# Optimization experiments

Hardware: AMD Instinct MI355X
Metric: run time of the kernel (lower is better)

## Reference

```python
import jax, jax.numpy as jnp
import numpy as np

K = 3       # kernel size
PAD = 1     # k // 2
S = 1       # stride
EPS = 1e-5  # BatchNorm eps


def setup_inputs() -> dict:
    key = jax.random.key(0)
    ks = jax.random.split(key, 7)
    B, C1, C2, H, W = 4, 256, 256, 80, 80
    x = jax.random.normal(ks[0], (B, C1, H, W), dtype=jnp.float32)
    # offset/mask conv params (orig inits these to zero; use small random so
    # the deformable sampling path is actually exercised)
    w_off = jax.random.normal(ks[1], (3 * K * K, C1, K, K), dtype=jnp.float32) * 0.01
    b_off = jax.random.normal(ks[2], (3 * K * K,), dtype=jnp.float32) * 0.01
    weight = jax.random.normal(ks[3], (C2, C1, K, K), dtype=jnp.float32) * 0.05
    bias = jax.random.normal(ks[4], (C2,), dtype=jnp.float32) * 0.05
    gamma = jnp.ones((C2,), dtype=jnp.float32)
    beta = jnp.zeros((C2,), dtype=jnp.float32)
    return {"x": x, "w_off": w_off, "b_off": b_off, "weight": weight,
            "bias": bias, "gamma": gamma, "beta": beta}


def _elastic_head(x, w_off, b_off, weight, bias, gamma, beta):
    B, C, H, W = x.shape
    K2 = K * K
    # offset/mask predictor conv (stride 1, SAME padding -> output H x W)
    off_out = jax.lax.conv_general_dilated(
        x, w_off, (S, S), 'SAME',
        dimension_numbers=('NCHW', 'OIHW', 'NCHW')) + b_off[None, :, None, None]
    o1, o2, m = off_out[:, :K2], off_out[:, K2:2 * K2], off_out[:, 2 * K2:]
    mask = jax.nn.sigmoid(m)                                   # [B,K2,H,W]
    # torchvision layout: channel 2p = dy_p, 2p+1 = dx_p
    off = jnp.concatenate([o1, o2], axis=1).reshape(B, K2, 2, H, W)
    dy, dx = off[:, :, 0], off[:, :, 1]                        # [B,K2,H,W]
    # base sampling grid per kernel tap
    ii, jj = jnp.meshgrid(jnp.arange(K), jnp.arange(K), indexing='ij')
    ii = ii.reshape(K2)
    jj = jj.reshape(K2)
    base_y = (jnp.arange(H)[None, :] * S - PAD + ii[:, None]).astype(x.dtype)  # [K2,H]
    base_x = (jnp.arange(W)[None, :] * S - PAD + jj[:, None]).astype(x.dtype)  # [K2,W]
    ys = dy + base_y[None, :, :, None]                         # [B,K2,H,W]
    xs = dx + base_x[None, :, None, :]
    y0 = jnp.floor(ys)
    x0 = jnp.floor(xs)
    wy = ys - y0
    wx = xs - x0
    y0i = y0.astype(jnp.int32)
    x0i = x0.astype(jnp.int32)
    y1i = y0i + 1
    x1i = x0i + 1
    x_flat = x.reshape(B, C, H * W)

    def gather(yy, xx):
        valid = ((yy >= 0) & (yy < H) & (xx >= 0) & (xx < W)).astype(x.dtype)
        idx = jnp.clip(yy, 0, H - 1) * W + jnp.clip(xx, 0, W - 1)
        g = jax.vmap(lambda xf, ix: xf[:, ix])(x_flat, idx.reshape(B, -1))
        return g.reshape(B, C, K2, H, W) * valid[:, None]

    # bilinear sample with zero padding outside, accumulate corners
    patches = (gather(y0i, x0i) * ((1 - wy) * (1 - wx))[:, None]
               + gather(y0i, x1i) * ((1 - wy) * wx)[:, None]
               + gather(y1i, x0i) * (wy * (1 - wx))[:, None]
               + gather(y1i, x1i) * (wy * wx)[:, None])       # [B,C,K2,H,W]
    patches = patches * mask[:, None]                          # modulation
    # implicit GEMM of deform_conv2d
    out = jnp.einsum('bcphw,ocp->bohw', patches,
                     weight.reshape(weight.shape[0], C, K2)) + bias[None, :, None, None]
    # BatchNorm2d (training-mode batch stats, biased variance) + SiLU
    mean = out.mean(axis=(0, 2, 3))
    var = out.var(axis=(0, 2, 3))
    xn = (out - mean[None, :, None, None]) * jax.lax.rsqrt(var + EPS)[None, :, None, None]
    y_bn = xn * gamma[None, :, None, None] + beta[None, :, None, None]
    return y_bn * jax.nn.sigmoid(y_bn)


def reference(x, w_off, b_off, weight, bias, gamma, beta):
    return _elastic_head(x, w_off, b_off, weight, bias, gamma, beta)
```

## Files before the change

### kernel.cpp

```cpp
#include <hip/hip_runtime.h>
#include <math.h>

constexpr int Hc = 80, Wc = 80, Bn = 4, C1 = 256, C2 = 256;
constexpr int HWn = Hc * Wc;
constexpr int NPIX = Bn * HWn;
constexpr int OFFC = 27;
constexpr int KK   = 2304;

typedef short bf16x8 __attribute__((ext_vector_type(8)));
typedef float f32x4  __attribute__((ext_vector_type(4)));

__device__ __forceinline__ unsigned f2bf(float f) {
    unsigned u = __float_as_uint(f);
    return (u + 0x7FFF + ((u >> 16) & 1)) >> 16;
}

__device__ __forceinline__ unsigned packhi2(float v0, float v1) {
    unsigned h;
    asm("v_cvt_pk_bf16_f32 %0, %1, %2" : "=v"(h) : "v"(v0), "v"(v1));
    return h;
}

__device__ __forceinline__ void ub4(uint2 u, float f[4]) {
    f[0] = __uint_as_float(u.x << 16);
    f[1] = __uint_as_float(u.x & 0xffff0000u);
    f[2] = __uint_as_float(u.y << 16);
    f[3] = __uint_as_float(u.y & 0xffff0000u);
}

__global__ __launch_bounds__(256) void k_wprep(const float* __restrict__ weight,
                                               unsigned short* __restrict__ wB1)
{
    int e = blockIdx.x * 256 + threadIdx.x;
    int kin = e & 7;
    int oc  = (e >> 3) & 255;
    int kg  = (e >> 11) & 3;
    int s   = e >> 13;
    int p   = s >> 3, cc = s & 7;
    float w = weight[((size_t)oc * C1 + cc * 32 + kg * 8 + kin) * 9 + p];
    wB1[e] = (unsigned short)f2bf(w);
}

__global__ __launch_bounds__(256) void k_wobprep(const float* __restrict__ w_off,
                                                 unsigned short* __restrict__ wOB)
{
    int e = blockIdx.x * 256 + threadIdx.x;
    int k  = e & 31;
    int oc = (e >> 5) & 31;
    int s  = e >> 10;
    int p  = s >> 3, cc = s & 7;
    float v = 0.f;
    if (oc < 27) v = w_off[((size_t)oc * C1 + cc * 32 + k) * 9 + p];
    wOB[e] = (unsigned short)f2bf(v);
}

__global__ __launch_bounds__(256) void k_xtrans(const float* __restrict__ x,
                                                unsigned short* __restrict__ xTb)
{
    __shared__ float tile[32][33];
    int bid = blockIdx.x;
    int ct  = bid & 7;
    int hwt = (bid >> 3) % 200;
    int b   = bid / 1600;
    int c0  = ct * 32, hw0 = hwt * 32;
    int tid = threadIdx.x;
    int col = tid & 31, rw = tid >> 5;
    const float* xb = x + (size_t)b * C1 * HWn;
    #pragma unroll
    for (int k = 0; k < 4; ++k) {
        int r = rw + k * 8;
        tile[r][col] = xb[(size_t)(c0 + r) * HWn + hw0 + col];
    }
    __syncthreads();
    unsigned short* xob = xTb + ((size_t)b * HWn + hw0) * C1 + c0;
    #pragma unroll
    for (int k = 0; k < 4; ++k) {
        int r = rw + k * 8;
        xob[(size_t)r * C1 + col] = (unsigned short)f2bf(tile[col][r]);
    }
}

__global__ __launch_bounds__(256) void k_offmfma(const unsigned short* __restrict__ xTb,
                                                 const unsigned short* __restrict__ wOB,
                                                 const float* __restrict__ b_off,
                                                 float* __restrict__ off)
{
    int t  = threadIdx.x;
    int wv = t >> 6, lane = t & 63;
    int li = lane & 15, kg = lane >> 4;
    int mi = wv & 1;
    int nj = wv >> 1;

    int mtile = ((blockIdx.x & 7) * 100) + (blockIdx.x >> 3);
    int m0  = mtile * 32;
    int b   = m0 / HWn;
    int hw0 = m0 - b * HWn;
    int pxl = hw0 + mi * 16 + li;
    int h = pxl / Wc, w = pxl - h * Wc;

    const unsigned short* xb = xTb + (size_t)b * HWn * C1;

    f32x4 acc = (f32x4){0.f, 0.f, 0.f, 0.f};
    #pragma unroll
    for (int p = 0; p < 9; ++p) {
        int dh = p / 3 - 1, dw = p % 3 - 1;
        int hh = h + dh, ww = w + dw;
        bool valid = (hh >= 0 && hh < Hc && ww >= 0 && ww < Wc);
        int hwp = valid ? (hh * Wc + ww) : 0;
        const unsigned short* arow = xb + (size_t)hwp * C1 + kg * 8;
        const unsigned short* brow = wOB + ((size_t)(p * 8) * 32 + nj * 16 + li) * 32 + kg * 8;
        #pragma unroll
        for (int cc = 0; cc < 8; ++cc) {
            uint4 av = *(const uint4*)(arow + cc * 32);
            if (!valid) av = make_uint4(0, 0, 0, 0);
            uint4 bv = *(const uint4*)(brow + cc * 1024);
            acc = __builtin_amdgcn_mfma_f32_16x16x32_bf16(
                __builtin_bit_cast(bf16x8, av), __builtin_bit_cast(bf16x8, bv), acc, 0, 0, 0);
        }
    }
    int oc = nj * 16 + li;
    if (oc < OFFC) {
        float bs = b_off[oc];
        float4 v;
        v.x = acc[0] + bs; v.y = acc[1] + bs; v.z = acc[2] + bs; v.w = acc[3] + bs;
        int hwd = hw0 + mi * 16 + kg * 4;
        *(float4*)&off[((size_t)b * OFFC + oc) * HWn + hwd] = v;
    }
}

__global__ __launch_bounds__(256) void k_meta(const float* __restrict__ off,
                                              int* __restrict__ crdbuf,
                                              float4* __restrict__ w4buf)
{
    int pair = blockIdx.x * 256 + threadIdx.x;
    int px = pair / 9, p = pair - px * 9;
    int b  = px / HWn, hw = px - b * HWn;
    int h = hw / Wc, w = hw - h * Wc;
    int ii = p / 3, jj = p - ii * 3;

    const float* ob = off + (size_t)b * OFFC * HWn + hw;
    float dy = ob[(2 * p) * HWn];
    float dx = ob[(2 * p + 1) * HWn];
    float mv = ob[(18 + p) * HWn];
    float mask = 1.0f / (1.0f + expf(-mv));
    float ys = dy + (float)(h - 1 + ii);
    float xsv = dx + (float)(w - 1 + jj);
    float y0f = floorf(ys), x0f = floorf(xsv);
    float wy = ys - y0f, wx = xsv - x0f;
    int y0 = (int)y0f, x0 = (int)x0f;
    int y1 = y0 + 1, x1 = x0 + 1;
    float vy0 = (y0 >= 0 && y0 < Hc) ? 1.f : 0.f;
    float vy1 = (y1 >= 0 && y1 < Hc) ? 1.f : 0.f;
    float vx0 = (x0 >= 0 && x0 < Wc) ? 1.f : 0.f;
    float vx1 = (x1 >= 0 && x1 < Wc) ? 1.f : 0.f;
    float4 wv;
    wv.x = mask * (1.f - wy) * (1.f - wx) * vy0 * vx0;
    wv.y = mask * (1.f - wy) * wx         * vy0 * vx1;
    wv.z = mask * wy         * (1.f - wx) * vy1 * vx0;
    wv.w = mask * wy         * wx         * vy1 * vx1;
    int cy0 = min(max(y0, 0), Hc - 1), cy1 = min(max(y1, 0), Hc - 1);
    int cx0 = min(max(x0, 0), Wc - 1), cx1 = min(max(x1, 0), Wc - 1);
    crdbuf[pair] = cy0 | (cy1 << 8) | (cx0 << 16) | (cx1 << 24);
    w4buf[pair]  = wv;
}

__global__ __launch_bounds__(256) void k_gather(const unsigned short* __restrict__ xTb,
                                                const int* __restrict__ crdbuf,
                                                const float4* __restrict__ w4buf,
                                                unsigned short* __restrict__ Ahi)
{
    int t   = threadIdx.x;
    int wv  = t >> 6, l = t & 63;
    int xcd = blockIdx.x & 7;
    int blk = blockIdx.x >> 3;
    int wgl = (xcd * 400 + blk) * 4 + wv;
    int base = wgl * 18;

    #pragma unroll 2
    for (int i = 0; i < 18; ++i) {
        int pair = base + i;
        int px = pair / 9, p = pair - px * 9;
        int b  = px / HWn;
        int crd = crdbuf[pair];
        float4 w4 = w4buf[pair];
        int cy0 = crd & 255, cy1 = (crd >> 8) & 255;
        int cx0 = (crd >> 16) & 255, cx1 = (crd >> 24) & 255;
        const unsigned short* xt = xTb + (size_t)b * HWn * C1;
        uint2 u00 = ((const uint2*)&xt[(size_t)(cy0 * Wc + cx0) * C1])[l];
        uint2 u01 = ((const uint2*)&xt[(size_t)(cy0 * Wc + cx1) * C1])[l];
        uint2 u10 = ((const uint2*)&xt[(size_t)(cy1 * Wc + cx0) * C1])[l];
        uint2 u11 = ((const uint2*)&xt[(size_t)(cy1 * Wc + cx1) * C1])[l];
        float f00[4], f01[4], f10[4], f11[4];
        ub4(u00, f00); ub4(u01, f01); ub4(u10, f10); ub4(u11, f11);
        float v0 = fmaf(w4.x, f00[0], fmaf(w4.y, f01[0], fmaf(w4.z, f10[0], w4.w * f11[0])));
        float v1 = fmaf(w4.x, f00[1], fmaf(w4.y, f01[1], fmaf(w4.z, f10[1], w4.w * f11[1])));
        float v2 = fmaf(w4.x, f00[2], fmaf(w4.y, f01[2], fmaf(w4.z, f10[2], w4.w * f11[2])));
        float v3 = fmaf(w4.x, f00[3], fmaf(w4.y, f01[3], fmaf(w4.z, f10[3], w4.w * f11[3])));
        unsigned h0 = packhi2(v0, v1), h1 = packhi2(v2, v3);
        int s = p * 8 + (l >> 3);
        size_t aidx = ((size_t)s * NPIX + px) * 32 + 4 * (l & 7);
        *(uint2*)&Ahi[aidx] = make_uint2(h0, h1);
    }
}

__global__ __launch_bounds__(256) void k_dmfma(const unsigned short* __restrict__ Ahi,
                                               const unsigned short* __restrict__ wB1,
                                               const float* __restrict__ bias,
                                               float* __restrict__ out)
{
    __shared__ float Tb[32 * 33];

    int t  = threadIdx.x;
    int wv = t >> 6, lane = t & 63;
    int li = lane & 15, kg = lane >> 4;
    int nh = wv;

    int mtile = ((blockIdx.x & 7) * 100) + (blockIdx.x >> 3);
    int m0  = mtile * 32;
    int b   = m0 / HWn;
    int hw0 = m0 - b * HWn;
    int row0 = m0 + li;
    int row1 = m0 + 16 + li;

    const unsigned short* a0p = Ahi + (size_t)row0 * 32 + kg * 8;
    const unsigned short* a1p = Ahi + (size_t)row1 * 32 + kg * 8;
    const unsigned short* bp  = wB1 + (size_t)(kg * 256 + nh * 64 + li) * 8;

    auto loadA = [&](int s, uint4& h0, uint4& h1) {
        size_t o = (size_t)s * NPIX * 32;
        h0 = *(const uint4*)(a0p + o);
        h1 = *(const uint4*)(a1p + o);
    };
    auto loadB = [&](int s, uint4& b0, uint4& b1, uint4& b2, uint4& b3) {
        const unsigned short* q = bp + (size_t)s * 8192;
        b0 = *(const uint4*)(q);
        b1 = *(const uint4*)(q + 128);
        b2 = *(const uint4*)(q + 256);
        b3 = *(const uint4*)(q + 384);
    };

    f32x4 acc[2][4];
    #pragma unroll
    for (int m = 0; m < 2; ++m)
        #pragma unroll
        for (int n = 0; n < 4; ++n) acc[m][n] = (f32x4){0.f, 0.f, 0.f, 0.f};

    uint4 aA0, aA1, bA0, bA1, bA2, bA3;
    uint4 aB0, aB1, bB0, bB1, bB2, bB3;

    auto compute = [&](uint4& c0, uint4& c1, uint4& q0, uint4& q1, uint4& q2, uint4& q3) {
        bf16x8 a0 = __builtin_bit_cast(bf16x8, c0);
        bf16x8 a1 = __builtin_bit_cast(bf16x8, c1);
        __builtin_amdgcn_s_setprio(1);
        bf16x8 v;
        v = __builtin_bit_cast(bf16x8, q0);
        acc[0][0] = __builtin_amdgcn_mfma_f32_16x16x32_bf16(a0, v, acc[0][0], 0, 0, 0);
        acc[1][0] = __builtin_amdgcn_mfma_f32_16x16x32_bf16(a1, v, acc[1][0], 0, 0, 0);
        v = __builtin_bit_cast(bf16x8, q1);
        acc[0][1] = __builtin_amdgcn_mfma_f32_16x16x32_bf16(a0, v, acc[0][1], 0, 0, 0);
        acc[1][1] = __builtin_amdgcn_mfma_f32_16x16x32_bf16(a1, v, acc[1][1], 0, 0, 0);
        v = __builtin_bit_cast(bf16x8, q2);
        acc[0][2] = __builtin_amdgcn_mfma_f32_16x16x32_bf16(a0, v, acc[0][2], 0, 0, 0);
        acc[1][2] = __builtin_amdgcn_mfma_f32_16x16x32_bf16(a1, v, acc[1][2], 0, 0, 0);
        v = __builtin_bit_cast(bf16x8, q3);
        acc[0][3] = __builtin_amdgcn_mfma_f32_16x16x32_bf16(a0, v, acc[0][3], 0, 0, 0);
        acc[1][3] = __builtin_amdgcn_mfma_f32_16x16x32_bf16(a1, v, acc[1][3], 0, 0, 0);
        __builtin_amdgcn_s_setprio(0);
    };

    loadA(0, aA0, aA1); loadB(0, bA0, bA1, bA2, bA3);
    for (int s = 0; s < 72; s += 2) {
        loadA(s + 1, aB0, aB1); loadB(s + 1, bB0, bB1, bB2, bB3);
        __builtin_amdgcn_sched_barrier(0);
        asm volatile("s_waitcnt vmcnt(6)" ::: "memory");
        __builtin_amdgcn_sched_barrier(0);
        compute(aA0, aA1, bA0, bA1, bA2, bA3);
        if (s + 2 < 72) { loadA(s + 2, aA0, aA1); loadB(s + 2, bA0, bA1, bA2, bA3); }
        __builtin_amdgcn_sched_barrier(0);
        if (s + 2 < 72) { asm volatile("s_waitcnt vmcnt(6)" ::: "memory"); }
        else            { asm volatile("s_waitcnt vmcnt(0)" ::: "memory"); }
        __builtin_amdgcn_sched_barrier(0);
        compute(aB0, aB1, bB0, bB1, bB2, bB3);
    }

    #pragma unroll
    for (int q = 0; q < 8; ++q) {
        __syncthreads();
        if (nh == (q >> 1)) {
            #pragma unroll
            for (int jj = 0; jj < 2; ++jj) {
                int nt = (q & 1) * 2 + jj;
                #pragma unroll
                for (int m = 0; m < 2; ++m) {
                    f32x4 a = acc[m][nt];
                    int rrw = jj * 16 + li;
                    int col = m * 16 + kg * 4;
                    #pragma unroll
                    for (int r = 0; r < 4; ++r)
                        Tb[rrw * 33 + col + r] = a[r];
                }
            }
        }
        __syncthreads();
        int px = t & 31;
        int rw = t >> 5;
        #pragma unroll
        for (int it = 0; it < 4; ++it) {
            int r  = it * 8 + rw;
            int oc = q * 32 + r;
            out[(size_t)(b * C2 + oc) * HWn + hw0 + px] = Tb[r * 33 + px] + bias[oc];
        }
    }
}

__global__ __launch_bounds__(256) void k_bnpart(const float* __restrict__ out,
                                                float* __restrict__ psum)
{
    int oc = blockIdx.x >> 2;
    int bq = blockIdx.x & 3;
    const float4* src = (const float4*)(out + ((size_t)(bq * C2 + oc)) * HWn);
    float s = 0.f, ss = 0.f;
    for (int i = threadIdx.x; i < 1600; i += 256) {
        float4 v = src[i];
        s  += v.x + v.y + v.z + v.w;
        ss += v.x * v.x + v.y * v.y + v.z * v.z + v.w * v.w;
    }
    __shared__ float ls[256], lss[256];
    ls[threadIdx.x] = s; lss[threadIdx.x] = ss;
    __syncthreads();
    for (int st = 128; st > 0; st >>= 1) {
        if (threadIdx.x < st) {
            ls[threadIdx.x]  += ls[threadIdx.x + st];
            lss[threadIdx.x] += lss[threadIdx.x + st];
        }
        __syncthreads();
    }
    if (threadIdx.x == 0) {
        atomicAdd(&psum[oc], ls[0]);
        atomicAdd(&psum[256 + oc], lss[0]);
    }
}

__global__ __launch_bounds__(256) void k_bnfin(const float* __restrict__ psum,
                                               float* __restrict__ stats)
{
    int oc = threadIdx.x;
    float mean = psum[oc] / (float)NPIX;
    float var  = psum[256 + oc] / (float)NPIX - mean * mean;
    stats[oc]       = mean;
    stats[256 + oc] = rsqrtf(var + 1e-5f);
}

__global__ __launch_bounds__(256) void k_bnsilu(float* __restrict__ out,
                                                const float* __restrict__ stats,
                                                const float* __restrict__ gamma,
                                                const float* __restrict__ beta)
{
    int n4 = (Bn * C2 * HWn) / 4;
    for (int i = blockIdx.x * blockDim.x + threadIdx.x; i < n4;
         i += gridDim.x * blockDim.x) {
        float4 v = ((float4*)out)[i];
        int e  = i * 4;
        int oc = (e / HWn) & 255;
        float mean = stats[oc];
        float gs   = gamma[oc] * stats[256 + oc];
        float bt   = beta[oc];
        float y;
        y = (v.x - mean) * gs + bt; v.x = y / (1.f + expf(-y));
        y = (v.y - mean) * gs + bt; v.y = y / (1.f + expf(-y));
        y = (v.z - mean) * gs + bt; v.z = y / (1.f + expf(-y));
        y = (v.w - mean) * gs + bt; v.w = y / (1.f + expf(-y));
        ((float4*)out)[i] = v;
    }
}

extern "C" void kernel_launch(void* const* d_in, const int* in_sizes, int n_in,
                              void* d_out, int out_size, void* d_ws, size_t ws_size,
                              hipStream_t stream)
{
    const float* x      = (const float*)d_in[0];
    const float* w_off  = (const float*)d_in[1];
    const float* b_off  = (const float*)d_in[2];
    const float* weight = (const float*)d_in[3];
    const float* bias   = (const float*)d_in[4];
    const float* gamma  = (const float*)d_in[5];
    const float* beta   = (const float*)d_in[6];
    float* out = (float*)d_out;

    char* wsb = (char*)d_ws;
    unsigned short* Ahi  = (unsigned short*)(wsb);
    unsigned short* xTb  = (unsigned short*)(wsb + 117964800);
    float*          off  = (float*)(wsb + 131072000);
    unsigned short* wB1  = (unsigned short*)(wsb + 133836800);
    unsigned short* wOB  = (unsigned short*)(wsb + 135016448);
    int*            crdb = (int*)(wsb + 135163904);
    float4*         w4b  = (float4*)(wsb + 136085504);
    float*         stats = (float*)(wsb + 139771904);
    float*         psum  = (float*)(wsb + 139773952);

    hipMemsetAsync(psum, 0, 2048, stream);
    k_wprep    <<<2304, 256, 0, stream>>>(weight, wB1);
    k_wobprep  <<<288, 256, 0, stream>>>(w_off, wOB);
    k_xtrans   <<<6400, 256, 0, stream>>>(x, xTb);
    k_offmfma  <<<800, 256, 0, stream>>>(xTb, wOB, b_off, off);
    k_meta     <<<900, 256, 0, stream>>>(off, crdb, w4b);
    k_gather   <<<3200, 256, 0, stream>>>(xTb, crdb, w4b, Ahi);
    k_dmfma    <<<800, 256, 0, stream>>>(Ahi, wB1, bias, out);
    k_bnpart   <<<1024, 256, 0, stream>>>(out, psum);
    k_bnfin    <<<1, 256, 0, stream>>>(psum, stats);
    k_bnsilu   <<<2048, 256, 0, stream>>>(out, stats, gamma, beta);
}
```

Measured before the change: 211.7 us.

## Fuse weight prep and offset/meta kernels, drop atomics and manual waitcnts

Merges the two weight-prep kernels into one launch and fuses the offset-conv MFMA with the sampling-metadata computation through shared memory, so the offset tensor never makes a round trip through global memory. The memset and atomic BN partial sums are replaced by per-batch partial slots that k_bnfin sums directly. The hand-placed s_waitcnt and sched_barrier in the main deform GEMM loop are removed, leaving scheduling to the compiler. These cut launches and memory traffic, at the risk of worse load/compute overlap in the GEMM.

```diff
diff --git a/kernel.cpp b/kernel.cpp
--- a/kernel.cpp
+++ b/kernel.cpp
@@ -28,30 +28,30 @@
     f[3] = __uint_as_float(u.y & 0xffff0000u);
 }
 
-__global__ __launch_bounds__(256) void k_wprep(const float* __restrict__ weight,
-                                               unsigned short* __restrict__ wB1)
-{
-    int e = blockIdx.x * 256 + threadIdx.x;
-    int kin = e & 7;
-    int oc  = (e >> 3) & 255;
-    int kg  = (e >> 11) & 3;
-    int s   = e >> 13;
-    int p   = s >> 3, cc = s & 7;
-    float w = weight[((size_t)oc * C1 + cc * 32 + kg * 8 + kin) * 9 + p];
-    wB1[e] = (unsigned short)f2bf(w);
-}
-
-__global__ __launch_bounds__(256) void k_wobprep(const float* __restrict__ w_off,
-                                                 unsigned short* __restrict__ wOB)
-{
-    int e = blockIdx.x * 256 + threadIdx.x;
-    int k  = e & 31;
-    int oc = (e >> 5) & 31;
-    int s  = e >> 10;
-    int p  = s >> 3, cc = s & 7;
-    float v = 0.f;
-    if (oc < 27) v = w_off[((size_t)oc * C1 + cc * 32 + k) * 9 + p];
-    wOB[e] = (unsigned short)f2bf(v);
+__global__ __launch_bounds__(256) void k_wprep2(const float* __restrict__ weight,
+                                                const float* __restrict__ w_off,
+                                                unsigned short* __restrict__ wB1,
+                                                unsigned short* __restrict__ wOB)
+{
+    if (blockIdx.x < 2304) {
+        int e = blockIdx.x * 256 + threadIdx.x;
+        int kin = e & 7;
+        int oc  = (e >> 3) & 255;
+        int kg  = (e >> 11) & 3;
+        int s   = e >> 13;
+        int p   = s >> 3, cc = s & 7;
+        float w = weight[((size_t)oc * C1 + cc * 32 + kg * 8 + kin) * 9 + p];
+        wB1[e] = (unsigned short)f2bf(w);
+    } else {
+        int e = (blockIdx.x - 2304) * 256 + threadIdx.x;
+        int k  = e & 31;
+        int oc = (e >> 5) & 31;
+        int s  = e >> 10;
+        int p  = s >> 3, cc = s & 7;
+        float v = 0.f;
+        if (oc < 27) v = w_off[((size_t)oc * C1 + cc * 32 + k) * 9 + p];
+        wOB[e] = (unsigned short)f2bf(v);
+    }
 }
 
 __global__ __launch_bounds__(256) void k_xtrans(const float* __restrict__ x,
@@ -80,11 +80,14 @@
     }
 }
 
-__global__ __launch_bounds__(256) void k_offmfma(const unsigned short* __restrict__ xTb,
+__global__ __launch_bounds__(256) void k_offmeta(const unsigned short* __restrict__ xTb,
                                                  const unsigned short* __restrict__ wOB,
                                                  const float* __restrict__ b_off,
-                                                 float* __restrict__ off)
-{
+                                                 int* __restrict__ crdbuf,
+                                                 float4* __restrict__ w4buf)
+{
+    __shared__ float offs[32][28];
+
     int t  = threadIdx.x;
     int wv = t >> 6, lane = t & 63;
     int li = lane & 15, kg = lane >> 4;
@@ -121,47 +124,42 @@
     int oc = nj * 16 + li;
     if (oc < OFFC) {
         float bs = b_off[oc];
-        float4 v;
-        v.x = acc[0] + bs; v.y = acc[1] + bs; v.z = acc[2] + bs; v.w = acc[3] + bs;
-        int hwd = hw0 + mi * 16 + kg * 4;
-        *(float4*)&off[((size_t)b * OFFC + oc) * HWn + hwd] = v;
-    }
-}
-
-__global__ __launch_bounds__(256) void k_meta(const float* __restrict__ off,
-                                              int* __restrict__ crdbuf,
-                                              float4* __restrict__ w4buf)
-{
-    int pair = blockIdx.x * 256 + threadIdx.x;
-    int px = pair / 9, p = pair - px * 9;
-    int b  = px / HWn, hw = px - b * HWn;
-    int h = hw / Wc, w = hw - h * Wc;
-    int ii = p / 3, jj = p - ii * 3;
-
-    const float* ob = off + (size_t)b * OFFC * HWn + hw;
-    float dy = ob[(2 * p) * HWn];
-    float dx = ob[(2 * p + 1) * HWn];
-    float mv = ob[(18 + p) * HWn];
-    float mask = 1.0f / (1.0f + expf(-mv));
-    float ys = dy + (float)(h - 1 + ii);
-    float xsv = dx + (float)(w - 1 + jj);
-    float y0f = floorf(ys), x0f = floorf(xsv);
-    float wy = ys - y0f, wx = xsv - x0f;
-    int y0 = (int)y0f, x0 = (int)x0f;
-    int y1 = y0 + 1, x1 = x0 + 1;
-    float vy0 = (y0 >= 0 && y0 < Hc) ? 1.f : 0.f;
-    float vy1 = (y1 >= 0 && y1 < Hc) ? 1.f : 0.f;
-    float vx0 = (x0 >= 0 && x0 < Wc) ? 1.f : 0.f;
-    float vx1 = (x1 >= 0 && x1 < Wc) ? 1.f : 0.f;
-    float4 wv;
-    wv.x = mask * (1.f - wy) * (1.f - wx) * vy0 * vx0;
-    wv.y = mask * (1.f - wy) * wx         * vy0 * vx1;
-    wv.z = mask * wy         * (1.f - wx) * vy1 * vx0;
-    wv.w = mask * wy         * wx         * vy1 * vx1;
-    int cy0 = min(max(y0, 0), Hc - 1), cy1 = min(max(y1, 0), Hc - 1);
-    int cx0 = min(max(x0, 0), Wc - 1), cx1 = min(max(x1, 0), Wc - 1);
-    crdbuf[pair] = cy0 | (cy1 << 8) | (cx0 << 16) | (cx1 << 24);
-    w4buf[pair]  = wv;
+        #pragma unroll
+        for (int r = 0; r < 4; ++r)
+            offs[mi * 16 + kg * 4 + r][oc] = acc[r] + bs;
+    }
+    __syncthreads();
+
+    for (int idx = t; idx < 288; idx += 256) {
+        int pix = idx / 9, p = idx - pix * 9;
+        int hw  = hw0 + pix;
+        int hh = hw / Wc, wwp = hw - hh * Wc;
+        int ii = p / 3, jj = p - ii * 3;
+        float dy = offs[pix][2 * p];
+        float dx = offs[pix][2 * p + 1];
+        float mv = offs[pix][18 + p];
+        float mask = 1.0f / (1.0f + expf(-mv));
+        float ys  = dy + (float)(hh - 1 + ii);
+        float xsv = dx + (float)(wwp - 1 + jj);
+        float y0f = floorf(ys), x0f = floorf(xsv);
+        float wy = ys - y0f, wx = xsv - x0f;
+        int y0 = (int)y0f, x0 = (int)x0f;
+        int y1 = y0 + 1, x1 = x0 + 1;
+        float vy0 = (y0 >= 0 && y0 < Hc) ? 1.f : 0.f;
+        float vy1 = (y1 >= 0 && y1 < Hc) ? 1.f : 0.f;
+        float vx0 = (x0 >= 0 && x0 < Wc) ? 1.f : 0.f;
+        float vx1 = (x1 >= 0 && x1 < Wc) ? 1.f : 0.f;
+        float4 wv4;
+        wv4.x = mask * (1.f - wy) * (1.f - wx) * vy0 * vx0;
+        wv4.y = mask * (1.f - wy) * wx         * vy0 * vx1;
+        wv4.z = mask * wy         * (1.f - wx) * vy1 * vx0;
+        wv4.w = mask * wy         * wx         * vy1 * vx1;
+        int cy0 = min(max(y0, 0), Hc - 1), cy1 = min(max(y1, 0), Hc - 1);
+        int cx0 = min(max(x0, 0), Wc - 1), cx1 = min(max(x1, 0), Wc - 1);
+        int pair = (m0 + pix) * 9 + p;
+        crdbuf[pair] = cy0 | (cy1 << 8) | (cx0 << 16) | (cx1 << 24);
+        w4buf[pair]  = wv4;
+    }
 }
 
 __global__ __launch_bounds__(256) void k_gather(const unsigned short* __restrict__ xTb,
@@ -271,15 +269,8 @@
     loadA(0, aA0, aA1); loadB(0, bA0, bA1, bA2, bA3);
     for (int s = 0; s < 72; s += 2) {
         loadA(s + 1, aB0, aB1); loadB(s + 1, bB0, bB1, bB2, bB3);
-        __builtin_amdgcn_sched_barrier(0);
-        asm volatile("s_waitcnt vmcnt(6)" ::: "memory");
-        __builtin_amdgcn_sched_barrier(0);
         compute(aA0, aA1, bA0, bA1, bA2, bA3);
         if (s + 2 < 72) { loadA(s + 2, aA0, aA1); loadB(s + 2, bA0, bA1, bA2, bA3); }
-        __builtin_amdgcn_sched_barrier(0);
-        if (s + 2 < 72) { asm volatile("s_waitcnt vmcnt(6)" ::: "memory"); }
-        else            { asm volatile("s_waitcnt vmcnt(0)" ::: "memory"); }
-        __builtin_amdgcn_sched_barrier(0);
         compute(aB0, aB1, bB0, bB1, bB2, bB3);
     }
 
@@ -336,8 +327,8 @@
         __syncthreads();
     }
     if (threadIdx.x == 0) {
-        atomicAdd(&psum[oc], ls[0]);
-        atomicAdd(&psum[256 + oc], lss[0]);
+        psum[bq * 256 + oc]        = ls[0];
+        psum[1024 + bq * 256 + oc] = lss[0];
     }
 }
 
@@ -345,8 +336,10 @@
                                                float* __restrict__ stats)
 {
     int oc = threadIdx.x;
-    float mean = psum[oc] / (float)NPIX;
-    float var  = psum[256 + oc] / (float)NPIX - mean * mean;
+    float s  = psum[oc] + psum[256 + oc] + psum[512 + oc] + psum[768 + oc];
+    float ss = psum[1024 + oc] + psum[1280 + oc] + psum[1536 + oc] + psum[1792 + oc];
+    float mean = s / (float)NPIX;
+    float var  = ss / (float)NPIX - mean * mean;
     stats[oc]       = mean;
     stats[256 + oc] = rsqrtf(var + 1e-5f);
 }
@@ -390,23 +383,19 @@
     char* wsb = (char*)d_ws;
     unsigned short* Ahi  = (unsigned short*)(wsb);
     unsigned short* xTb  = (unsigned short*)(wsb + 117964800);
-    float*          off  = (float*)(wsb + 131072000);
-    unsigned short* wB1  = (unsigned short*)(wsb + 133836800);
-    unsigned short* wOB  = (unsigned short*)(wsb + 135016448);
-    int*            crdb = (int*)(wsb + 135163904);
-    float4*         w4b  = (float4*)(wsb + 136085504);
-    float*         stats = (float*)(wsb + 139771904);
-    float*         psum  = (float*)(wsb + 139773952);
-
-    hipMemsetAsync(psum, 0, 2048, stream);
-    k_wprep    <<<2304, 256, 0, stream>>>(weight, wB1);
-    k_wobprep  <<<288, 256, 0, stream>>>(w_off, wOB);
-    k_xtrans   <<<6400, 256, 0, stream>>>(x, xTb);
-    k_offmfma  <<<800, 256, 0, stream>>>(xTb, wOB, b_off, off);
-    k_meta     <<<900, 256, 0, stream>>>(off, crdb, w4b);
-    k_gather   <<<3200, 256, 0, stream>>>(xTb, crdb, w4b, Ahi);
-    k_dmfma    <<<800, 256, 0, stream>>>(Ahi, wB1, bias, out);
-    k_bnpart   <<<1024, 256, 0, stream>>>(out, psum);
-    k_bnfin    <<<1, 256, 0, stream>>>(psum, stats);
-    k_bnsilu   <<<2048, 256, 0, stream>>>(out, stats, gamma, beta);
-}
+    unsigned short* wB1  = (unsigned short*)(wsb + 131072000);
+    unsigned short* wOB  = (unsigned short*)(wsb + 132251648);
+    int*            crdb = (int*)(wsb + 132399104);
+    float4*         w4b  = (float4*)(wsb + 133320704);
+    float*         stats = (float*)(wsb + 137007104);
+    float*         psum  = (float*)(wsb + 137009152);
+
+    k_wprep2  <<<2592, 256, 0, stream>>>(weight, w_off, wB1, wOB);
+    k_xtrans  <<<6400, 256, 0, stream>>>(x, xTb);
+    k_offmeta <<<800, 256, 0, stream>>>(xTb, wOB, b_off, crdb, w4b);
+    k_gather  <<<3200, 256, 0, stream>>>(xTb, crdb, w4b, Ahi);
+    k_dmfma   <<<800, 256, 0, stream>>>(Ahi, wB1, bias, out);
+    k_bnpart  <<<1024, 256, 0, stream>>>(out, psum);
+    k_bnfin   <<<1, 256, 0, stream>>>(psum, stats);
+    k_bnsilu  <<<2048, 256, 0, stream>>>(out, stats, gamma, beta);
+}
```

New measurement: 202.5 us, median of 2. 4.3% less time.
